# Kernel tuning notes

Measured on AMD Instinct MI355X. Metric: run time of the kernel, lower is better.

The kernel has to match this reference:

```python
import jax, jax.numpy as jnp
import numpy as np

STRIDE, PAD, DIL = 1, 1, 1


def setup_inputs() -> dict:
    key = jax.random.key(0)
    k1, k2, k3, k4, k5 = jax.random.split(key, 5)
    N, Cin, H, W = 8, 256, 64, 64
    Cout, K = 256, 3
    x = jax.random.normal(k1, (N, Cin, H, W), dtype=jnp.float32)
    offset = jax.random.normal(k2, (N, 2 * K * K, H, W), dtype=jnp.float32)
    mask = jax.random.uniform(k3, (N, K * K, H, W), dtype=jnp.float32)
    weight = jax.random.normal(k4, (Cout, Cin, K, K), dtype=jnp.float32) * 0.02
    bias = jax.random.normal(k5, (Cout,), dtype=jnp.float32)
    return {"x": x, "offset": offset, "mask": mask, "weight": weight, "bias": bias}


def _gather(im_flat, idx):
    # im_flat: (N, Goff, Cg, H*W); idx: (N, Goff, KK, Ho, Wo) int32
    # -> (N, Goff, Cg, KK, Ho, Wo)
    f = lambda imf, ix: imf[:, ix]
    return jax.vmap(jax.vmap(f))(im_flat, idx)


def _deform_conv2d(x, offset, mask, weight, bias):
    N, Cin, H, W = x.shape
    Cout, Cin_g, Kh, Kw = weight.shape
    KK = Kh * Kw
    Goff = offset.shape[1] // (2 * KK)
    Ho = (H + 2 * PAD - (DIL * (Kh - 1) + 1)) // STRIDE + 1
    Wo = (W + 2 * PAD - (DIL * (Kw - 1) + 1)) // STRIDE + 1

    # base sampling grid per kernel tap: (KK, Ho, Wo)
    py = (jnp.arange(Kh)[:, None] * DIL + jnp.arange(Ho)[None, :] * STRIDE - PAD).astype(jnp.float32)
    px = (jnp.arange(Kw)[:, None] * DIL + jnp.arange(Wo)[None, :] * STRIDE - PAD).astype(jnp.float32)
    y_base = jnp.broadcast_to(py[:, None, :, None], (Kh, Kw, Ho, Wo)).reshape(KK, Ho, Wo)
    x_base = jnp.broadcast_to(px[None, :, None, :], (Kh, Kw, Ho, Wo)).reshape(KK, Ho, Wo)

    off = offset.reshape(N, Goff, KK, 2, Ho, Wo)  # [...,0]=dy, [...,1]=dx
    ys = y_base[None, None] + off[:, :, :, 0]  # (N, Goff, KK, Ho, Wo)
    xs = x_base[None, None] + off[:, :, :, 1]

    Cg = Cin // Goff
    im_flat = x.reshape(N, Goff, Cg, H * W)

    y0 = jnp.floor(ys)
    x0 = jnp.floor(xs)
    acc = jnp.zeros((N, Goff, Cg, KK, Ho, Wo), dtype=x.dtype)
    for dy in (0.0, 1.0):
        for dx in (0.0, 1.0):
            yi = y0 + dy
            xi = x0 + dx
            wgt = (1.0 - jnp.abs(ys - yi)) * (1.0 - jnp.abs(xs - xi))
            valid = (yi >= 0) & (yi < H) & (xi >= 0) & (xi < W)
            idx = (jnp.clip(yi, 0, H - 1) * W + jnp.clip(xi, 0, W - 1)).astype(jnp.int32)
            g = _gather(im_flat, idx)  # (N,Goff,Cg,KK,Ho,Wo)
            acc = acc + g * (wgt * valid.astype(x.dtype))[:, :, None]

    m = mask.reshape(N, Goff, KK, Ho, Wo)
    sampled = acc * m[:, :, None]  # DCNv2 modulation

    # grouped conv accumulate as GEMM over (Cin_g*KK)
    gw = Cin // Cin_g
    cols = sampled.reshape(N, gw, Cin_g * KK, Ho * Wo)
    wflat = weight.reshape(gw, Cout // gw, Cin_g * KK)
    out = jnp.einsum('goc,ngcl->ngol', wflat, cols).reshape(N, Cout, Ho, Wo)
    return out + bias[None, :, None, None]


def reference(x, offset, mask, weight, bias):
    return _deform_conv2d(x, offset, mask, weight, bias)
```

## Files before the change

### kernel.cpp

```cpp
#include <hip/hip_runtime.h>
#include <stdint.h>

typedef unsigned int u32;
typedef unsigned short u16;
typedef float f32x4 __attribute__((ext_vector_type(4)));
typedef __fp16 h16x2 __attribute__((ext_vector_type(2)));
typedef _Float16 f16x8 __attribute__((ext_vector_type(8)));
typedef float f4u __attribute__((ext_vector_type(4), aligned(4)));

#define NB   8
#define CIN  256
#define HH   64
#define WW   64
#define HW   4096
#define COUT 256
#define BSTR 264

__device__ __forceinline__ u32 pkh(float lo, float hi) {
  h16x2 h = __builtin_amdgcn_cvt_pkrtz(lo, hi);
  return __builtin_bit_cast(u32, h);
}
union HU { u32 u; h16x2 h; };

__global__ __launch_bounds__(256) void prep_all(const float* __restrict__ x,
                                                const float* __restrict__ wgt,
                                                u32* __restrict__ xT,
                                                u32* __restrict__ W2f32) {
  int b = blockIdx.x;
  int t = threadIdx.x;
  if (b < 512) {
    __shared__ u32 tile[64][129];
    int n = b >> 6, hw0 = (b & 63) << 6;
    int hw4 = (t & 15) << 2;
    int cp0 = t >> 4;
    const float* xb = x + (size_t)n * CIN * HW + hw0 + hw4;
#pragma unroll
    for (int it = 0; it < 8; ++it) {
      int cp = (it << 4) + cp0;
      int c = cp << 1;
      f4u v0 = *(const f4u*)(xb + (size_t)c * HW);
      f4u v1 = *(const f4u*)(xb + (size_t)(c + 1) * HW);
      tile[hw4 + 0][cp] = pkh(v0.x, v1.x);
      tile[hw4 + 1][cp] = pkh(v0.y, v1.y);
      tile[hw4 + 2][cp] = pkh(v0.z, v1.z);
      tile[hw4 + 3][cp] = pkh(v0.w, v1.w);
    }
    __syncthreads();
    u32* outp = xT + ((size_t)(n * HW + hw0)) * 128;
    int cp = t & 127, hb = t >> 7;
#pragma unroll
    for (int it = 0; it < 32; ++it) {
      int hwl = (it << 1) + hb;
      outp[(size_t)hwl * 128 + cp] = tile[hwl][cp];
    }
  } else {
    int tt = (b - 512) * 256 + t;
    int cp = tt & 127, co = tt >> 7;
    int c = cp << 1;
    const float* p = wgt + ((size_t)co * CIN + c) * 9;
    f4u q0 = *(const f4u*)(p + 0);
    f4u q1 = *(const f4u*)(p + 4);
    f4u q2 = *(const f4u*)(p + 8);
    f4u q3 = *(const f4u*)(p + 12);
    float e16 = p[16], e17 = p[17];
    float a0[9], a1[9];
    a0[0]=q0.x; a0[1]=q0.y; a0[2]=q0.z; a0[3]=q0.w;
    a0[4]=q1.x; a0[5]=q1.y; a0[6]=q1.z; a0[7]=q1.w; a0[8]=q2.x;
    a1[0]=q2.y; a1[1]=q2.z; a1[2]=q2.w;
    a1[3]=q3.x; a1[4]=q3.y; a1[5]=q3.z; a1[6]=q3.w; a1[7]=e16; a1[8]=e17;
    int cc = c >> 5;
    int j = (c >> 1) & 3;
    int lane = (co & 15) | (((c >> 3) & 3) << 4);
    int tile_ = ((co >> 6) << 2) | ((co >> 4) & 3);
#pragma unroll
    for (int kk = 0; kk < 9; ++kk) {
      int frag = (kk * 8 + cc) * 16 + tile_;
      W2f32[(size_t)frag * 256 + lane * 4 + j] = pkh(a0[kk], a1[kk]);
    }
  }
}

__global__ __launch_bounds__(512, 4) void dcn_main(
    const float* __restrict__ offset, const float* __restrict__ mask,
    const float* __restrict__ bias, const u16* __restrict__ xT,
    const u16* __restrict__ W2f, float* __restrict__ out) {
  __shared__ __align__(16) u16 Bs[2][64 * BSTR];
  __shared__ __align__(8)  uint2 swl[576];
  __shared__ __align__(8)  ushort4 sol[576];

  int bid = blockIdx.x;
  int n = bid & 7;
  int ho = bid >> 3;
  int t = threadIdx.x;
  int lane = t & 63;
  int w = t >> 6;

  for (int i = t; i < 576; i += 512) {
    int kk = i >> 6, p = i & 63;
    int ky = kk / 3, kx = kk - ky * 3;
    int sp = (ho << 6) + p;
    float dy = offset[(((size_t)n * 18 + kk * 2 + 0) << 12) + sp];
    float dx = offset[(((size_t)n * 18 + kk * 2 + 1) << 12) + sp];
    float m  = mask  [(((size_t)n * 9  + kk) << 12) + sp];
    float ys = (float)(ky + ho - 1) + dy;
    float xs = (float)(kx + p  - 1) + dx;
    float y0f = floorf(ys), x0f = floorf(xs);
    float fy = ys - y0f, fx = xs - x0f;
    int y0 = (int)y0f, x0 = (int)x0f;
    int y1 = y0 + 1, x1 = x0 + 1;
    float vy0 = (y0 >= 0 && y0 < HH) ? 1.f : 0.f;
    float vy1 = (y1 >= 0 && y1 < HH) ? 1.f : 0.f;
    float vx0 = (x0 >= 0 && x0 < WW) ? 1.f : 0.f;
    float vx1 = (x1 >= 0 && x1 < WW) ? 1.f : 0.f;
    float w0 = (1.f - fy) * (1.f - fx) * m * vy0 * vx0;
    float w1 = (1.f - fy) * fx * m * vy0 * vx1;
    float w2 = fy * (1.f - fx) * m * vy1 * vx0;
    float w3 = fy * fx * m * vy1 * vx1;
    int iy0 = min(max(y0, 0), HH - 1), iy1 = min(max(y1, 0), HH - 1);
    int ix0 = min(max(x0, 0), WW - 1), ix1 = min(max(x1, 0), WW - 1);
    ushort4 pv;
    pv.x = (u16)((iy0 << 6) + ix0);
    pv.y = (u16)((iy0 << 6) + ix1);
    pv.z = (u16)((iy1 << 6) + ix0);
    pv.w = (u16)((iy1 << 6) + ix1);
    swl[i] = make_uint2(pkh(w0, w1), pkh(w2, w3));
    sol[i] = pv;
  }
  __syncthreads();

  f32x4 acc[2][4];
#pragma unroll
  for (int a = 0; a < 2; ++a)
#pragma unroll
    for (int b2 = 0; b2 < 4; ++b2) acc[a][b2] = {0.f, 0.f, 0.f, 0.f};

  const char* xTn = (const char*)xT + ((size_t)n * HW << 9);
  int ml = lane & 15, q = lane >> 4;
  int hwid = t >> 5;
  int l32 = t & 31;
  int tile0 = ((w >> 1) << 2) + ((w & 1) << 1);
  const char* bch = xTn + (l32 << 4);

#define CORNER(P, WT) do {                                             \
    uint4 qv = *(const uint4*)(bch + ((int)(P) << 9));                 \
    float wt = (WT);                                                   \
    HU h0, h1, h2, h3;                                                 \
    h0.u = qv.x; h1.u = qv.y; h2.u = qv.z; h3.u = qv.w;                \
    s0 = __builtin_fmaf((float)h0.h.x, wt, s0);                        \
    s1 = __builtin_fmaf((float)h0.h.y, wt, s1);                        \
    s2 = __builtin_fmaf((float)h1.h.x, wt, s2);                        \
    s3 = __builtin_fmaf((float)h1.h.y, wt, s3);                        \
    s4 = __builtin_fmaf((float)h2.h.x, wt, s4);                        \
    s5 = __builtin_fmaf((float)h2.h.y, wt, s5);                        \
    s6 = __builtin_fmaf((float)h3.h.x, wt, s6);                        \
    s7 = __builtin_fmaf((float)h3.h.y, wt, s7);                        \
  } while (0)

  auto build = [&](int kk, int i, int buf) {
    int px = (i << 4) + hwid;
    uint2 wu = swl[(kk << 6) + px];
    ushort4 pv = sol[(kk << 6) + px];
    HU ha, hb; ha.u = wu.x; hb.u = wu.y;
    float w0 = (float)ha.h.x, w1 = (float)ha.h.y;
    float w2 = (float)hb.h.x, w3 = (float)hb.h.y;
    float s0=0.f,s1=0.f,s2=0.f,s3=0.f,s4=0.f,s5=0.f,s6=0.f,s7=0.f;
    CORNER(pv.x, w0);
    CORNER(pv.y, w1);
    CORNER(pv.z, w2);
    CORNER(pv.w, w3);
    uint4 pkd;
    pkd.x = pkh(s0, s1); pkd.y = pkh(s2, s3);
    pkd.z = pkh(s4, s5); pkd.w = pkh(s6, s7);
    *(uint4*)((char*)&Bs[buf][0] + px * (BSTR * 2) + (l32 << 4)) = pkd;
  };

#pragma unroll
  for (int i = 0; i < 4; ++i) build(0, i, 0);
  __syncthreads();

#pragma unroll 1
  for (int kk = 0; kk < 9; ++kk) {
    int cur = kk & 1;
#pragma unroll
    for (int g = 0; g < 4; ++g) {
      if (kk < 8) build(kk + 1, g, cur ^ 1);
#pragma unroll
      for (int c2 = 0; c2 < 2; ++c2) {
        int cc = (g << 1) | c2;
        f16x8 af[2], bf[4];
#pragma unroll
        for (int mt = 0; mt < 2; ++mt)
          af[mt] = *(const f16x8*)(W2f +
                   (((size_t)((kk * 8 + cc) * 16 + tile0 + mt)) << 9) + (lane << 3));
#pragma unroll
        for (int nt = 0; nt < 4; ++nt)
          bf[nt] = *(const f16x8*)((const char*)&Bs[cur][0] +
                   ((nt << 4) + ml) * (BSTR * 2) + (cc << 6) + (q << 4));
#pragma unroll
        for (int mt = 0; mt < 2; ++mt)
#pragma unroll
          for (int nt = 0; nt < 4; ++nt)
            acc[mt][nt] = __builtin_amdgcn_mfma_f32_16x16x32_f16(af[mt], bf[nt],
                                                                 acc[mt][nt], 0, 0, 0);
      }
    }
    __syncthreads();
  }

  size_t obase = ((size_t)n * COUT) * HW + ((size_t)ho << 6);
#pragma unroll
  for (int mt = 0; mt < 2; ++mt) {
#pragma unroll
    for (int r = 0; r < 4; ++r) {
      int co = (w << 5) + (mt << 4) + (q << 2) + r;
      float bv = bias[co];
#pragma unroll
      for (int nt = 0; nt < 4; ++nt) {
        int wo = (nt << 4) + ml;
        out[obase + (size_t)co * HW + wo] = acc[mt][nt][r] + bv;
      }
    }
  }
}

extern "C" void kernel_launch(void* const* d_in, const int* in_sizes, int n_in,
                              void* d_out, int out_size, void* d_ws, size_t ws_size,
                              hipStream_t stream) {
  const float* x      = (const float*)d_in[0];
  const float* offset = (const float*)d_in[1];
  const float* mask   = (const float*)d_in[2];
  const float* weight = (const float*)d_in[3];
  const float* bias   = (const float*)d_in[4];
  float* out = (float*)d_out;

  u16* xT  = (u16*)d_ws;
  u16* W2f = (u16*)((char*)d_ws + (size_t)NB * HW * CIN * 2);

  prep_all<<<640, 256, 0, stream>>>(x, weight, (u32*)xT, (u32*)W2f);
  dcn_main<<<512, 512, 0, stream>>>(offset, mask, bias, xT, W2f, out);
}
```

Baseline: 148.8 us.

## Overlap gather loads and weight fragment prefetch with MFMA compute

```diff
diff --git a/kernel.cpp b/kernel.cpp
--- a/kernel.cpp
+++ b/kernel.cpp
@@ -141,11 +141,10 @@
   int tile0 = ((w >> 1) << 2) + ((w & 1) << 1);
   const char* bch = xTn + (l32 << 4);
 
-#define CORNER(P, WT) do {                                             \
-    uint4 qv = *(const uint4*)(bch + ((int)(P) << 9));                 \
+#define CMB(G, WT) do {                                                \
     float wt = (WT);                                                   \
     HU h0, h1, h2, h3;                                                 \
-    h0.u = qv.x; h1.u = qv.y; h2.u = qv.z; h3.u = qv.w;                \
+    h0.u = (G).x; h1.u = (G).y; h2.u = (G).z; h3.u = (G).w;            \
     s0 = __builtin_fmaf((float)h0.h.x, wt, s0);                        \
     s1 = __builtin_fmaf((float)h0.h.y, wt, s1);                        \
     s2 = __builtin_fmaf((float)h1.h.x, wt, s2);                        \
@@ -156,52 +155,92 @@
     s7 = __builtin_fmaf((float)h3.h.y, wt, s7);                        \
   } while (0)
 
-  auto build = [&](int kk, int i, int buf) {
+  auto build0 = [&](int i) {
     int px = (i << 4) + hwid;
-    uint2 wu = swl[(kk << 6) + px];
-    ushort4 pv = sol[(kk << 6) + px];
+    uint2 wu = swl[px];
+    ushort4 pv = sol[px];
     HU ha, hb; ha.u = wu.x; hb.u = wu.y;
-    float w0 = (float)ha.h.x, w1 = (float)ha.h.y;
-    float w2 = (float)hb.h.x, w3 = (float)hb.h.y;
+    uint4 G0 = *(const uint4*)(bch + ((int)pv.x << 9));
+    uint4 G1 = *(const uint4*)(bch + ((int)pv.y << 9));
+    uint4 G2 = *(const uint4*)(bch + ((int)pv.z << 9));
+    uint4 G3 = *(const uint4*)(bch + ((int)pv.w << 9));
     float s0=0.f,s1=0.f,s2=0.f,s3=0.f,s4=0.f,s5=0.f,s6=0.f,s7=0.f;
-    CORNER(pv.x, w0);
-    CORNER(pv.y, w1);
-    CORNER(pv.z, w2);
-    CORNER(pv.w, w3);
+    CMB(G0, (float)ha.h.x);
+    CMB(G1, (float)ha.h.y);
+    CMB(G2, (float)hb.h.x);
+    CMB(G3, (float)hb.h.y);
     uint4 pkd;
     pkd.x = pkh(s0, s1); pkd.y = pkh(s2, s3);
     pkd.z = pkh(s4, s5); pkd.w = pkh(s6, s7);
-    *(uint4*)((char*)&Bs[buf][0] + px * (BSTR * 2) + (l32 << 4)) = pkd;
+    *(uint4*)((char*)&Bs[0][0] + px * (BSTR * 2) + (l32 << 4)) = pkd;
   };
 
-#pragma unroll
-  for (int i = 0; i < 4; ++i) build(0, i, 0);
+  auto af_load = [&](int fidx, int mt) {
+    return *(const f16x8*)(W2f +
+           (((size_t)((fidx << 4) + tile0 + mt)) << 9) + (lane << 3));
+  };
+
+#pragma unroll
+  for (int i = 0; i < 4; ++i) build0(i);
   __syncthreads();
+
+  f16x8 afc0 = af_load(0, 0);
+  f16x8 afc1 = af_load(0, 1);
 
 #pragma unroll 1
   for (int kk = 0; kk < 9; ++kk) {
     int cur = kk & 1;
+    char* Bw = (char*)&Bs[cur ^ 1][0];
+    const char* Br = (const char*)&Bs[cur][0];
+    int fbase = kk << 3;
 #pragma unroll
     for (int g = 0; g < 4; ++g) {
-      if (kk < 8) build(kk + 1, g, cur ^ 1);
+      int px = (g << 4) + hwid;
+      uint4 G0, G1, G2, G3;
+      float cw0, cw1, cw2, cw3;
+      if (kk < 8) {
+        int ii = ((kk + 1) << 6) + px;
+        uint2 wu = swl[ii];
+        ushort4 pv = sol[ii];
+        HU ha, hb; ha.u = wu.x; hb.u = wu.y;
+        cw0 = (float)ha.h.x; cw1 = (float)ha.h.y;
+        cw2 = (float)hb.h.x; cw3 = (float)hb.h.y;
+        G0 = *(const uint4*)(bch + ((int)pv.x << 9));
+        G1 = *(const uint4*)(bch + ((int)pv.y << 9));
+        G2 = *(const uint4*)(bch + ((int)pv.z << 9));
+        G3 = *(const uint4*)(bch + ((int)pv.w << 9));
+      }
 #pragma unroll
       for (int c2 = 0; c2 < 2; ++c2) {
         int cc = (g << 1) | c2;
-        f16x8 af[2], bf[4];
-#pragma unroll
-        for (int mt = 0; mt < 2; ++mt)
-          af[mt] = *(const f16x8*)(W2f +
-                   (((size_t)((kk * 8 + cc) * 16 + tile0 + mt)) << 9) + (lane << 3));
+        int nf = fbase + cc + 1; if (nf > 71) nf = 71;
+        f16x8 afn0 = af_load(nf, 0);
+        f16x8 afn1 = af_load(nf, 1);
+        f16x8 bf[4];
 #pragma unroll
         for (int nt = 0; nt < 4; ++nt)
-          bf[nt] = *(const f16x8*)((const char*)&Bs[cur][0] +
-                   ((nt << 4) + ml) * (BSTR * 2) + (cc << 6) + (q << 4));
-#pragma unroll
-        for (int mt = 0; mt < 2; ++mt)
-#pragma unroll
-          for (int nt = 0; nt < 4; ++nt)
-            acc[mt][nt] = __builtin_amdgcn_mfma_f32_16x16x32_f16(af[mt], bf[nt],
-                                                                 acc[mt][nt], 0, 0, 0);
+          bf[nt] = *(const f16x8*)(Br + ((nt << 4) + ml) * (BSTR * 2) +
+                                   (cc << 6) + (q << 4));
+#pragma unroll
+        for (int nt = 0; nt < 4; ++nt)
+          acc[0][nt] = __builtin_amdgcn_mfma_f32_16x16x32_f16(afc0, bf[nt],
+                                                              acc[0][nt], 0, 0, 0);
+#pragma unroll
+        for (int nt = 0; nt < 4; ++nt)
+          acc[1][nt] = __builtin_amdgcn_mfma_f32_16x16x32_f16(afc1, bf[nt],
+                                                              acc[1][nt], 0, 0, 0);
+        afc0 = afn0; afc1 = afn1;
+      }
+      if (kk < 8) {
+        float s0=0.f,s1=0.f,s2=0.f,s3=0.f,s4=0.f,s5=0.f,s6=0.f,s7=0.f;
+        CMB(G0, cw0);
+        CMB(G1, cw1);
+        CMB(G2, cw2);
+        CMB(G3, cw3);
+        uint4 pkd;
+        pkd.x = pkh(s0, s1); pkd.y = pkh(s2, s3);
+        pkd.z = pkh(s4, s5); pkd.w = pkh(s6, s7);
+        *(uint4*)(Bw + px * (BSTR * 2) + (l32 << 4)) = pkd;
       }
     }
     __syncthreads();
```

Measured after the change: 144.6 us. 2.8% less time.
